# Performance work log

Hardware: AMD Instinct MI355X
Metric: run time of the kernel (lower is better)

## Reference

```python
import jax, jax.numpy as jnp
import numpy as np
import math

B, S, E, H = 2, 8192, 1024, 16
D = E // H  # 64
CHUNK = 128


def _build_slopes(n):
    # ALiBi-style slopes (n is a power of 2 here)
    start = 2.0 ** (-(2.0 ** -(math.log2(n) - 3)))
    return np.array([start * (start ** i) for i in range(n)], dtype=np.float32)


def setup_inputs() -> dict:
    key = jax.random.key(0)
    ks = jax.random.split(key, 6)
    x = jax.random.normal(ks[0], (B, S, E), dtype=jnp.float32)
    # rotary table: (S, D//2, 2) = (cos, sin)
    inv_freq = 1.0 / (10000.0 ** (np.arange(0, D, 2, dtype=np.float32) / D))
    ang = np.arange(S, dtype=np.float32)[:, None] * inv_freq[None, :]  # (S, D/2)
    freqs_cis = jnp.asarray(np.stack([np.cos(ang), np.sin(ang)], axis=-1))
    wq = jax.random.normal(ks[1], (E, E), dtype=jnp.float32) * 0.02
    wk = jax.random.normal(ks[2], (E, E), dtype=jnp.float32) * 0.02
    wv = jax.random.normal(ks[3], (E, E), dtype=jnp.float32) * 0.02
    wo = jax.random.normal(ks[4], (E, E), dtype=jnp.float32) * 0.02
    rms_w = jnp.ones((E,), dtype=jnp.float32)
    return {"x": x, "freqs_cis": freqs_cis, "wq": wq, "wk": wk, "wv": wv, "wo": wo, "rms_w": rms_w}


def apply_rotary(x, fc):
    # x: (b, s, h, d); fc: (s, d/2, 2)
    xr = x.reshape(*x.shape[:-1], -1, 2)          # (b,s,h,d/2,2)
    fc = fc[None, :, None, :, :]                   # (1,s,1,d/2,2)
    out = jnp.stack([
        xr[..., 0] * fc[..., 0] - xr[..., 1] * fc[..., 1],
        xr[..., 1] * fc[..., 0] + xr[..., 0] * fc[..., 1],
    ], axis=-1)
    return out.reshape(x.shape)


def lightning_attn(q, k, v, slopes, C=CHUNK):
    # q,k,v: (B,H,S,D); per-head decay lambda = exp(-slope)
    Bs, Hs, Ss, Ds = q.shape
    NC = Ss // C
    j = jnp.arange(C, dtype=jnp.float32)
    diff = j[:, None] - j[None, :]
    s3 = slopes[:, None, None]                     # (H,1,1)
    Dmask = jnp.where(diff >= 0, jnp.exp(-s3 * diff), 0.0)   # (H,C,C) intra decay
    q_dec = jnp.exp(-slopes[:, None] * (j + 1.0))             # (H,C) cross-chunk q decay
    k_dec = jnp.exp(-slopes[:, None] * (C - 1.0 - j))         # (H,C) state-update k decay
    c_dec = jnp.exp(-slopes * C)[None, :, None, None]         # (1,H,1,1) full-chunk decay
    qc = q.reshape(Bs, Hs, NC, C, Ds).transpose(2, 0, 1, 3, 4)
    kc = k.reshape(Bs, Hs, NC, C, Ds).transpose(2, 0, 1, 3, 4)
    vc = v.reshape(Bs, Hs, NC, C, Ds).transpose(2, 0, 1, 3, 4)

    def step(St, inp):
        qb, kb, vb = inp                                       # (B,H,C,D)
        scores = jnp.einsum('bhid,bhjd->bhij', qb, kb) * Dmask[None]
        o = jnp.einsum('bhij,bhjd->bhid', scores, vb)
        o = o + q_dec[None, :, :, None] * jnp.einsum('bhid,bhde->bhie', qb, St)
        St = c_dec * St + jnp.einsum('bhcd,bhce->bhde', kb * k_dec[None, :, :, None], vb)
        return St, o

    S0 = jnp.zeros((Bs, Hs, Ds, Ds), dtype=jnp.float32)
    _, oc = jax.lax.scan(step, S0, (qc, kc, vc))               # oc: (NC,B,H,C,D)
    return oc.transpose(1, 2, 0, 3, 4).reshape(Bs, Hs, Ss, Ds)


def rms_norm(x, w, eps=1e-5):
    xf = x.astype(jnp.float32)
    n = xf * jax.lax.rsqrt(jnp.mean(xf * xf, axis=-1, keepdims=True) + eps)
    return n.astype(x.dtype) * w


def reference(x, freqs_cis, wq, wk, wv, wo, rms_w):
    b, s, _ = x.shape
    slopes = jnp.asarray(_build_slopes(H))
    q = (x @ wq.T).reshape(b, s, H, D)
    k = (x @ wk.T).reshape(b, s, H, D)
    v = (x @ wv.T).reshape(b, s, H, D)
    q = apply_rotary(q, freqs_cis)
    k = apply_rotary(k, freqs_cis)
    q = q.transpose(0, 2, 1, 3)   # (B,H,S,D)
    k = k.transpose(0, 2, 1, 3)
    v = v.transpose(0, 2, 1, 3)
    o = lightning_attn(q, k, v, slopes)             # (B,H,S,D)
    o = o.transpose(0, 2, 1, 3).reshape(b, s, E)    # b n (h d)
    o = rms_norm(o, rms_w)
    return o @ wo.T
```

## Files before the change

kernel.cpp:

```cpp
#include <hip/hip_runtime.h>


using h16   = _Float16;
using h16x8 = __attribute__((ext_vector_type(8))) _Float16;
using h16x4 = __attribute__((ext_vector_type(4))) _Float16;
using f32x4 = __attribute__((ext_vector_type(4))) float;

#define MFMA16(a,b,c) __builtin_amdgcn_mfma_f32_16x16x32_f16(a,b,c,0,0,0)

#define GLOAD16(gp, lp) __builtin_amdgcn_global_load_lds( \
    (const __attribute__((address_space(1))) void*)(gp),  \
    (__attribute__((address_space(3))) void*)(lp), 16, 0, 0)

__device__ __forceinline__ h16x8 rope8(h16x8 v, const float* __restrict__ fp) {
  float4 f0 = *(const float4*)fp;
  float4 f1 = *(const float4*)(fp + 4);
  h16x8 o; float x0, x1;
  x0=(float)v[0]; x1=(float)v[1]; o[0]=(h16)(x0*f0.x - x1*f0.y); o[1]=(h16)(x1*f0.x + x0*f0.y);
  x0=(float)v[2]; x1=(float)v[3]; o[2]=(h16)(x0*f0.z - x1*f0.w); o[3]=(h16)(x1*f0.z + x0*f0.w);
  x0=(float)v[4]; x1=(float)v[5]; o[4]=(h16)(x0*f1.x - x1*f1.y); o[5]=(h16)(x1*f1.x + x0*f1.y);
  x0=(float)v[6]; x1=(float)v[7]; o[6]=(h16)(x0*f1.z - x1*f1.w); o[7]=(h16)(x1*f1.z + x0*f1.w);
  return o;
}

__global__ __launch_bounds__(256) void k_cvt(const float* __restrict__ s,
                                             h16* __restrict__ d, int n) {
  int i = (blockIdx.x * 256 + threadIdx.x) * 8;
  if (i >= n) return;
  float4 a = *(const float4*)(s + i);
  float4 b = *(const float4*)(s + i + 4);
  h16x8 o;
  o[0]=(h16)a.x; o[1]=(h16)a.y; o[2]=(h16)a.z; o[3]=(h16)a.w;
  o[4]=(h16)b.x; o[5]=(h16)b.y; o[6]=(h16)b.z; o[7]=(h16)b.w;
  *(h16x8*)(d + i) = o;
}

__device__ __forceinline__ void gemm256_loop(
    const h16* __restrict__ At, const h16* __restrict__ Bt,
    char* smem, int w, int l, f32x4 (&acc)[8][4])
{
  char* lA = smem;
  char* lB = smem + 65536;
  const int wr = w >> 2, wc = w & 3;
  const int rl = l >> 3;
  const int sl8 = ((l & 7) ^ rl) * 8;

  auto stage = [&](int kt) {
    const int kb = (kt & 1) * 32768;
    #pragma unroll
    for (int half = 0; half < 2; half++) {
      #pragma unroll
      for (int c = 0; c < 2; c++) {
        const int r = half*128 + (c*8 + w)*8 + rl;
        const int dof = kb + half*16384 + (c*8 + w)*1024;
        GLOAD16(At + (size_t)r*1024 + kt*64 + sl8, lA + dof);
        GLOAD16(Bt + (size_t)r*1024 + kt*64 + sl8, lB + dof);
      }
    }
  };

  const int foff0 = (((l >> 4)    ) ^ (l & 7)) * 16;
  const int foff1 = (((l >> 4) + 4) ^ (l & 7)) * 16;
  const int abyte = wr*16384 + (l & 15)*128;
  const int bbyte = (wc >> 1)*16384 + ((wc & 1)*64 + (l & 15))*128;

  stage(0); stage(1);
  asm volatile("s_waitcnt vmcnt(8)" ::: "memory");
  __builtin_amdgcn_sched_barrier(0);
  __builtin_amdgcn_s_barrier();

  for (int t = 0; t < 16; ++t) {
    const int kb = (t & 1) * 32768;
    const char* aB = lA + kb + abyte;
    const char* bB = lB + kb + bbyte;
    h16x8 af0[8], af1[8], bf0[4], bf1[4];
    #pragma unroll
    for (int mf = 0; mf < 8; mf++) {
      af0[mf] = *(const h16x8*)(aB + mf*2048 + foff0);
      af1[mf] = *(const h16x8*)(aB + mf*2048 + foff1);
    }
    #pragma unroll
    for (int nf = 0; nf < 4; nf++) {
      bf0[nf] = *(const h16x8*)(bB + nf*2048 + foff0);
      bf1[nf] = *(const h16x8*)(bB + nf*2048 + foff1);
    }
    asm volatile("s_waitcnt lgkmcnt(0)" ::: "memory");
    __builtin_amdgcn_sched_barrier(0);
    __builtin_amdgcn_s_barrier();
    if (t < 14) stage(t + 2);
    __builtin_amdgcn_s_setprio(1);
    #pragma unroll
    for (int mf = 0; mf < 8; mf++)
      #pragma unroll
      for (int nf = 0; nf < 4; nf++)
        acc[mf][nf] = MFMA16(af0[mf], bf0[nf], acc[mf][nf]);
    #pragma unroll
    for (int mf = 0; mf < 8; mf++)
      #pragma unroll
      for (int nf = 0; nf < 4; nf++)
        acc[mf][nf] = MFMA16(af1[mf], bf1[nf], acc[mf][nf]);
    __builtin_amdgcn_s_setprio(0);
    if (t < 14)       asm volatile("s_waitcnt vmcnt(8)" ::: "memory");
    else if (t == 14) asm volatile("s_waitcnt vmcnt(0)" ::: "memory");
    if (t < 15) {
      __builtin_amdgcn_sched_barrier(0);
      __builtin_amdgcn_s_barrier();
    }
  }
}

__global__ __launch_bounds__(512, 2) void k_qkv(
    const h16* __restrict__ xh, const h16* __restrict__ w3,
    h16* __restrict__ qn, h16* __restrict__ kn, h16* __restrict__ vn)
{
  extern __shared__ __align__(16) char smem[];
  const int tid = threadIdx.x;
  const int w = tid >> 6, l = tid & 63;
  const int m0 = blockIdx.x * 256;
  const int nt = blockIdx.y;
  const int wr = w >> 2, wc = w & 3;

  f32x4 acc[8][4] = {};
  gemm256_loop(xh + (size_t)m0*1024, w3 + (size_t)(nt*256)*1024, smem, w, l, acc);

  const int proj = nt >> 2;
  h16* dst = proj == 0 ? qn : (proj == 1 ? kn : vn);
  const int cb = (nt & 3)*256 + wc*64;
  #pragma unroll
  for (int mf = 0; mf < 8; mf++)
    #pragma unroll
    for (int nf = 0; nf < 4; nf++)
      #pragma unroll
      for (int r = 0; r < 4; r++) {
        int row = wr*128 + mf*16 + ((l >> 4) << 2) + r;
        int col = cb + nf*16 + (l & 15);
        dst[(size_t)(m0 + row)*1024 + col] = (h16)acc[mf][nf][r];
      }
}

__global__ __launch_bounds__(512, 2) void k_out(
    const h16* __restrict__ an, const h16* __restrict__ woh,
    float* __restrict__ out)
{
  extern __shared__ __align__(16) char smem[];
  const int tid = threadIdx.x;
  const int w = tid >> 6, l = tid & 63;
  const int m0 = blockIdx.x * 256;
  const int n0 = blockIdx.y * 256;
  const int wr = w >> 2, wc = w & 3;

  f32x4 acc[8][4] = {};
  gemm256_loop(an + (size_t)m0*1024, woh + (size_t)n0*1024, smem, w, l, acc);

  #pragma unroll
  for (int mf = 0; mf < 8; mf++)
    #pragma unroll
    for (int nf = 0; nf < 4; nf++)
      #pragma unroll
      for (int r = 0; r < 4; r++) {
        int row = wr*128 + mf*16 + ((l >> 4) << 2) + r;
        int col = n0 + wc*64 + nf*16 + (l & 15);
        out[(size_t)(m0 + row)*1024 + col] = acc[mf][nf][r];
      }
}

__global__ __launch_bounds__(256) void k_tr(
    const h16* __restrict__ kn, const h16* __restrict__ vn,
    const float* __restrict__ fc,
    h16* __restrict__ kts, h16* __restrict__ vt)
{
  __shared__ __align__(16) h16 tl[128*64];
  __shared__ float dt[128];
  const int tid = threadIdx.x;
  const int st = blockIdx.x;
  const int bh = blockIdx.y;
  const int b = bh >> 4, h = bh & 15;
  if (tid < 128) {
    float slope = exp2f(-0.5f * (float)(h + 1));
    dt[tid] = expf(-slope * (float)(127 - tid));
  }
  const size_t ibase = ((size_t)(b*8192 + st*128))*1024 + h*64;
  const size_t obase = (size_t)bh*64*8192 + st*128;
  const int cr = tid >> 3, c8 = tid & 7;

  for (int which = 0; which < 2; ++which) {
    const h16* src = which ? vn : kn;
    h16* dstp = which ? vt : kts;
    __syncthreads();
    #pragma unroll
    for (int i = 0; i < 4; i++) {
      int r = i*32 + cr;
      h16x8 v = *(const h16x8*)(src + ibase + (size_t)r*1024 + c8*8);
      if (!which) v = rope8(v, fc + (size_t)(st*128 + r)*64 + c8*8);
      int slot = (c8 + ((r >> 3) & 7)) & 7;
      *(h16x8*)(tl + r*64 + slot*8) = v;
    }
    __syncthreads();
    #pragma unroll
    for (int i = 0; i < 4; i++) {
      int chunk = i*256 + tid;
      int d = chunk >> 4;
      int j8 = chunk & 15;
      h16x8 o;
      #pragma unroll
      for (int jj = 0; jj < 8; jj++) {
        int c = j8*8 + jj;
        int pos = (d + ((c >> 3) & 7)*8) & 63;
        float fv = (float)tl[c*64 + pos];
        if (!which) fv *= dt[c];
        o[jj] = (h16)fv;
      }
      *(h16x8*)(dstp + obase + (size_t)d*8192 + j8*8) = o;
    }
  }
}

__global__ __launch_bounds__(256) void k_kv(
    const h16* __restrict__ kts, const h16* __restrict__ vt,
    float* __restrict__ T)
{
  const int tid = threadIdx.x;
  const int t = blockIdx.x;
  const int bh = blockIdx.y;
  const int w = tid >> 6, l = tid & 63;
  const h16* vb = vt  + (size_t)bh*64*8192 + t*128;
  const h16* kb = kts + (size_t)bh*64*8192 + t*128;
  f32x4 acc[4] = {};
  h16x8 a[4];
  #pragma unroll
  for (int ks = 0; ks < 4; ks++)
    a[ks] = *(const h16x8*)(vb + (size_t)(w*16 + (l & 15))*8192 + ks*32 + (l >> 4)*8);
  #pragma unroll
  for (int nf = 0; nf < 4; nf++) {
    #pragma unroll
    for (int ks = 0; ks < 4; ks++) {
      h16x8 bfr = *(const h16x8*)(kb + (size_t)(nf*16 + (l & 15))*8192 + ks*32 + (l >> 4)*8);
      acc[nf] = MFMA16(a[ks], bfr, acc[nf]);
    }
  }
  float* Tb = T + ((size_t)bh*64 + t)*4096;
  #pragma unroll
  for (int nf = 0; nf < 4; nf++)
    #pragma unroll
    for (int r = 0; r < 4; r++) {
      int e = w*16 + ((l >> 4) << 2) + r;
      int d = nf*16 + (l & 15);
      Tb[e*64 + d] = acc[nf][r];
    }
}

__global__ __launch_bounds__(256) void k_scan(const float* __restrict__ T,
                                              h16* __restrict__ ph) {
  const int bh = blockIdx.x;
  const int j  = blockIdx.y * 256 + threadIdx.x;
  const int h = bh & 15;
  const float cdec = expf(-exp2f(-0.5f*(float)(h+1)) * 128.0f);
  const float* Tb = T + (size_t)bh*64*4096 + j;
  h16* pb = ph + (size_t)bh*64*4096 + j;
  float run = 0.f;
  for (int t = 0; t < 64; t++) {
    float kv = Tb[(size_t)t*4096];
    pb[(size_t)t*4096] = (h16)run;
    run = cdec*run + kv;
  }
}

__global__ __launch_bounds__(256) void k_att(
    const h16* __restrict__ qn, const h16* __restrict__ kn,
    const float* __restrict__ fc,
    const h16* __restrict__ vt, const h16* __restrict__ ph,
    h16* __restrict__ oh)
{
  __shared__ __align__(16) h16 P[128*144];
  __shared__ float dt[128], qd[128];
  const int tid = threadIdx.x;
  const int t = blockIdx.x;
  const int bh = blockIdx.y;
  const int b = bh >> 4, h = bh & 15;
  if (tid < 128) {
    float slope = exp2f(-0.5f*(float)(h+1));
    dt[tid] = expf(-slope*(float)tid);
    qd[tid] = expf(-slope*(float)(tid+1));
  }
  __syncthreads();
  const int w = tid >> 6, l = tid & 63;
  const int iw = w * 32;
  const h16* qb = qn + ((size_t)(b*8192 + t*128))*1024 + h*64;
  const h16* kb = kn + ((size_t)(b*8192 + t*128))*1024 + h*64;
  const h16* vb = vt + (size_t)bh*64*8192 + t*128;
  const h16* pb = ph + ((size_t)bh*64 + t)*4096;
  const float* fcb = fc + (size_t)(t*128)*64;

  h16x8 aq[2][2];
  #pragma unroll
  for (int mf = 0; mf < 2; mf++)
    #pragma unroll
    for (int ks = 0; ks < 2; ks++) {
      int row = iw + mf*16 + (l & 15);
      int d0 = ks*32 + (l >> 4)*8;
      aq[mf][ks] = rope8(*(const h16x8*)(qb + (size_t)row*1024 + d0),
                         fcb + (size_t)row*64 + d0);
    }

  f32x4 sc[2][8] = {};
  #pragma unroll
  for (int nf = 0; nf < 8; nf++) {
    if (nf*16 <= iw + 31) {
      #pragma unroll
      for (int ks = 0; ks < 2; ks++) {
        int row = nf*16 + (l & 15);
        int d0 = ks*32 + (l >> 4)*8;
        h16x8 bk = rope8(*(const h16x8*)(kb + (size_t)row*1024 + d0),
                         fcb + (size_t)row*64 + d0);
        sc[0][nf] = MFMA16(aq[0][ks], bk, sc[0][nf]);
        sc[1][nf] = MFMA16(aq[1][ks], bk, sc[1][nf]);
      }
    }
  }
  #pragma unroll
  for (int mf = 0; mf < 2; mf++) {
    #pragma unroll
    for (int nf = 0; nf < 8; nf++) {
      #pragma unroll
      for (int r = 0; r < 4; r++) {
        int i = iw + mf*16 + ((l >> 4) << 2) + r;
        int j = nf*16 + (l & 15);
        int diff = i - j;
        float v = diff >= 0 ? sc[mf][nf][r]*dt[diff] : 0.f;
        P[i*144 + j] = (h16)v;
      }
    }
  }
  f32x4 ao[2][4] = {};
  #pragma unroll
  for (int kc = 0; kc < 4; kc++) {
    h16x8 ap0 = *(const h16x8*)(P + (size_t)(iw + (l & 15))*144 + kc*32 + (l >> 4)*8);
    h16x8 ap1 = *(const h16x8*)(P + (size_t)(iw + 16 + (l & 15))*144 + kc*32 + (l >> 4)*8);
    #pragma unroll
    for (int nf = 0; nf < 4; nf++) {
      h16x8 bv = *(const h16x8*)(vb + (size_t)(nf*16 + (l & 15))*8192 + kc*32 + (l >> 4)*8);
      ao[0][nf] = MFMA16(ap0, bv, ao[0][nf]);
      ao[1][nf] = MFMA16(ap1, bv, ao[1][nf]);
    }
  }
  f32x4 a2[2][4] = {};
  #pragma unroll
  for (int ks = 0; ks < 2; ks++) {
    #pragma unroll
    for (int nf = 0; nf < 4; nf++) {
      h16x8 bs = *(const h16x8*)(pb + (size_t)(nf*16 + (l & 15))*64 + ks*32 + (l >> 4)*8);
      a2[0][nf] = MFMA16(aq[0][ks], bs, a2[0][nf]);
      a2[1][nf] = MFMA16(aq[1][ks], bs, a2[1][nf]);
    }
  }
  #pragma unroll
  for (int mf = 0; mf < 2; mf++) {
    #pragma unroll
    for (int nf = 0; nf < 4; nf++) {
      #pragma unroll
      for (int r = 0; r < 4; r++) {
        int i = iw + mf*16 + ((l >> 4) << 2) + r;
        int e = nf*16 + (l & 15);
        float o = ao[mf][nf][r] + qd[i]*a2[mf][nf][r];
        int s = t*128 + i;
        oh[((size_t)(b*8192 + s))*1024 + h*64 + e] = (h16)o;
      }
    }
  }
}

__global__ __launch_bounds__(256) void k_rms(const h16* __restrict__ o,
                                             const float* __restrict__ rw,
                                             h16* __restrict__ an) {
  const int tid = threadIdx.x;
  const size_t base = (size_t)blockIdx.x * 1024;
  h16x4 hv = *(const h16x4*)(o + base + tid*4);
  float v0 = (float)hv[0], v1 = (float)hv[1], v2 = (float)hv[2], v3 = (float)hv[3];
  float ss = v0*v0 + v1*v1 + v2*v2 + v3*v3;
  #pragma unroll
  for (int off = 32; off > 0; off >>= 1) ss += __shfl_down(ss, off);
  __shared__ float red[4];
  if ((tid & 63) == 0) red[tid >> 6] = ss;
  __syncthreads();
  float f = rsqrtf((red[0]+red[1]+red[2]+red[3]) * (1.0f/1024.0f) + 1e-5f);
  float4 wv = *(const float4*)(rw + tid*4);
  h16x4 r;
  r[0] = (h16)(v0*f*wv.x); r[1] = (h16)(v1*f*wv.y);
  r[2] = (h16)(v2*f*wv.z); r[3] = (h16)(v3*f*wv.w);
  *(h16x4*)(an + base + tid*4) = r;
}

extern "C" void kernel_launch(void* const* d_in, const int* in_sizes, int n_in,
                              void* d_out, int out_size, void* d_ws, size_t ws_size,
                              hipStream_t stream) {
  const float* x  = (const float*)d_in[0];
  const float* fc = (const float*)d_in[1];
  const float* wq = (const float*)d_in[2];
  const float* wk = (const float*)d_in[3];
  const float* wv = (const float*)d_in[4];
  const float* wo = (const float*)d_in[5];
  const float* rw = (const float*)d_in[6];
  float* out = (float*)d_out;

  char* p = (char*)d_ws;
  const size_t SZ = 33554432;
  h16* xh  = (h16*)(p);
  h16* vn  = (h16*)(p + 3*SZ);
  h16* kts = (h16*)(p + 4*SZ);
  h16* vt  = (h16*)(p + 5*SZ);
  float* T = (float*)(p + 6*SZ);
  h16* w3  = (h16*)(p + 7*SZ);
  h16* woh = (h16*)(p + 7*SZ + 6291456);
  h16* qn = (h16*)out;
  h16* kn = (h16*)out + 16777216;

  (void)hipFuncSetAttribute((const void*)k_qkv, hipFuncAttributeMaxDynamicSharedMemorySize, 131072);
  (void)hipFuncSetAttribute((const void*)k_out, hipFuncAttributeMaxDynamicSharedMemorySize, 131072);

  hipLaunchKernelGGL(k_cvt, dim3(8192), dim3(256), 0, stream, x, xh, 16777216);
  hipLaunchKernelGGL(k_cvt, dim3(512), dim3(256), 0, stream, wq, w3, 1048576);
  hipLaunchKernelGGL(k_cvt, dim3(512), dim3(256), 0, stream, wk, w3 + 1048576, 1048576);
  hipLaunchKernelGGL(k_cvt, dim3(512), dim3(256), 0, stream, wv, w3 + 2097152, 1048576);
  hipLaunchKernelGGL(k_cvt, dim3(512), dim3(256), 0, stream, wo, woh, 1048576);

  hipLaunchKernelGGL(k_qkv, dim3(64, 12), dim3(512), 131072, stream, xh, w3, qn, kn, vn);
  hipLaunchKernelGGL(k_tr,  dim3(64, 32), dim3(256), 0, stream, kn, vn, fc, kts, vt);
  hipLaunchKernelGGL(k_kv,  dim3(64, 32), dim3(256), 0, stream, kts, vt, T);
  h16* ph = vn;
  hipLaunchKernelGGL(k_scan, dim3(32, 16), dim3(256), 0, stream, T, ph);
  h16* oh = (h16*)T;
  hipLaunchKernelGGL(k_att, dim3(64, 32), dim3(256), 0, stream, qn, kn, fc, vt, ph, oh);
  h16* an = xh;
  hipLaunchKernelGGL(k_rms, dim3(16384), dim3(256), 0, stream, oh, rw, an);
  hipLaunchKernelGGL(k_out, dim3(64, 4), dim3(512), 131072, stream, an, woh, out);
}
```

Measured before the change: 318.2 us.

## Restructure GEMM main loop to K=32 steps with quad-buffered LDS and split A/B staging

The 256x256 GEMM mainloop moves from 16 K-steps of 64 with double buffering to 32 K-steps of 32 with four LDS buffers. The global-to-LDS loads are split into separate A and B stages, each interleaved between two halves of the MFMA work, and the swizzle and fragment addressing change to match. The aim is finer-grained overlap of loads with MFMA and one fewer barrier per iteration. The cost is twice as many loop iterations and waits, and an altered LDS bank-conflict pattern that might not be conflict-free.

```diff
diff --git a/kernel.cpp b/kernel.cpp
--- a/kernel.cpp
+++ b/kernel.cpp
@@ -39,70 +39,72 @@
     const h16* __restrict__ At, const h16* __restrict__ Bt,
     char* smem, int w, int l, f32x4 (&acc)[8][4])
 {
-  char* lA = smem;
-  char* lB = smem + 65536;
+  const int tid = w*64 + l;
   const int wr = w >> 2, wc = w & 3;
-  const int rl = l >> 3;
-  const int sl8 = ((l & 7) ^ rl) * 8;
-
-  auto stage = [&](int kt) {
-    const int kb = (kt & 1) * 32768;
-    #pragma unroll
-    for (int half = 0; half < 2; half++) {
-      #pragma unroll
-      for (int c = 0; c < 2; c++) {
-        const int r = half*128 + (c*8 + w)*8 + rl;
-        const int dof = kb + half*16384 + (c*8 + w)*1024;
-        GLOAD16(At + (size_t)r*1024 + kt*64 + sl8, lA + dof);
-        GLOAD16(Bt + (size_t)r*1024 + kt*64 + sl8, lB + dof);
-      }
-    }
+
+  size_t gof[2];
+  #pragma unroll
+  for (int c = 0; c < 2; c++) {
+    int G = c*512 + tid;
+    int pp = G >> 3;
+    int idx = (G & 7) ^ (pp & 7);
+    gof[c] = (size_t)(2*pp + (idx >> 2))*1024 + (idx & 3)*8;
+  }
+
+  const int q16 = ((((l & 1) << 2) | (l >> 4)) ^ ((l >> 1) & 7)) * 16;
+  const int abyte = wr*8192 + ((l >> 1) & 7)*128 + q16;
+  const int bbyte = 16384 + wc*4096 + ((l >> 1) & 7)*128 + q16;
+
+  auto stageA = [&](int kt) {
+    char* buf = smem + (kt & 3)*32768;
+    #pragma unroll
+    for (int c = 0; c < 2; c++)
+      GLOAD16(At + gof[c] + kt*32, buf + c*8192 + w*1024);
   };
-
-  const int foff0 = (((l >> 4)    ) ^ (l & 7)) * 16;
-  const int foff1 = (((l >> 4) + 4) ^ (l & 7)) * 16;
-  const int abyte = wr*16384 + (l & 15)*128;
-  const int bbyte = (wc >> 1)*16384 + ((wc & 1)*64 + (l & 15))*128;
-
-  stage(0); stage(1);
-  asm volatile("s_waitcnt vmcnt(8)" ::: "memory");
+  auto stageB = [&](int kt) {
+    char* buf = smem + (kt & 3)*32768;
+    #pragma unroll
+    for (int c = 0; c < 2; c++)
+      GLOAD16(Bt + gof[c] + kt*32, buf + 16384 + c*8192 + w*1024);
+  };
+
+  stageA(0); stageB(0); stageA(1); stageB(1);
+  asm volatile("s_waitcnt vmcnt(4)" ::: "memory");
   __builtin_amdgcn_sched_barrier(0);
   __builtin_amdgcn_s_barrier();
 
-  for (int t = 0; t < 16; ++t) {
-    const int kb = (t & 1) * 32768;
-    const char* aB = lA + kb + abyte;
-    const char* bB = lB + kb + bbyte;
-    h16x8 af0[8], af1[8], bf0[4], bf1[4];
-    #pragma unroll
-    for (int mf = 0; mf < 8; mf++) {
-      af0[mf] = *(const h16x8*)(aB + mf*2048 + foff0);
-      af1[mf] = *(const h16x8*)(aB + mf*2048 + foff1);
-    }
-    #pragma unroll
-    for (int nf = 0; nf < 4; nf++) {
-      bf0[nf] = *(const h16x8*)(bB + nf*2048 + foff0);
-      bf1[nf] = *(const h16x8*)(bB + nf*2048 + foff1);
-    }
+  for (int t = 0; t < 32; ++t) {
+    const char* buf = smem + (t & 3)*32768;
+    h16x8 af[8], bf[4];
+    #pragma unroll
+    for (int mf = 0; mf < 4; mf++) af[mf] = *(const h16x8*)(buf + abyte + mf*1024);
+    #pragma unroll
+    for (int nf = 0; nf < 4; nf++) bf[nf] = *(const h16x8*)(buf + bbyte + nf*1024);
+    if (t < 30) stageA(t + 2);
     asm volatile("s_waitcnt lgkmcnt(0)" ::: "memory");
     __builtin_amdgcn_sched_barrier(0);
-    __builtin_amdgcn_s_barrier();
-    if (t < 14) stage(t + 2);
     __builtin_amdgcn_s_setprio(1);
     #pragma unroll
-    for (int mf = 0; mf < 8; mf++)
+    for (int mf = 0; mf < 4; mf++)
       #pragma unroll
       for (int nf = 0; nf < 4; nf++)
-        acc[mf][nf] = MFMA16(af0[mf], bf0[nf], acc[mf][nf]);
-    #pragma unroll
-    for (int mf = 0; mf < 8; mf++)
+        acc[mf][nf] = MFMA16(af[mf], bf[nf], acc[mf][nf]);
+    __builtin_amdgcn_s_setprio(0);
+    #pragma unroll
+    for (int mf = 0; mf < 4; mf++) af[4+mf] = *(const h16x8*)(buf + abyte + 4096 + mf*1024);
+    if (t < 30) stageB(t + 2);
+    asm volatile("s_waitcnt lgkmcnt(0)" ::: "memory");
+    __builtin_amdgcn_sched_barrier(0);
+    __builtin_amdgcn_s_setprio(1);
+    #pragma unroll
+    for (int mf = 0; mf < 4; mf++)
       #pragma unroll
       for (int nf = 0; nf < 4; nf++)
-        acc[mf][nf] = MFMA16(af1[mf], bf1[nf], acc[mf][nf]);
+        acc[4+mf][nf] = MFMA16(af[4+mf], bf[nf], acc[4+mf][nf]);
     __builtin_amdgcn_s_setprio(0);
-    if (t < 14)       asm volatile("s_waitcnt vmcnt(8)" ::: "memory");
-    else if (t == 14) asm volatile("s_waitcnt vmcnt(0)" ::: "memory");
-    if (t < 15) {
+    if (t < 30)       asm volatile("s_waitcnt vmcnt(4)" ::: "memory");
+    else if (t == 30) asm volatile("s_waitcnt vmcnt(0)" ::: "memory");
+    if (t < 31) {
       __builtin_amdgcn_sched_barrier(0);
       __builtin_amdgcn_s_barrier();
     }
```

New measurement: 327.0 us. +2.8%, slower.
